# Performance work log

Measured on AMD Instinct MI355X. Metric: run time of the kernel, lower is better.

Reference implementation:

```python
import jax, jax.numpy as jnp
import numpy as np

BN_EPS = 1e-5

def conv1x1(x, w, b):
    # x: [B,C,H,W], w: [O,C], b: [O]
    return jnp.einsum('bchw,oc->bohw', x, w) + b[None, :, None, None]

def maxpool2(x):
    B, C, H, W = x.shape
    return x.reshape(B, C, H // 2, 2, W // 2, 2).max(axis=(3, 5))

def setup_inputs() -> dict:
    key = jax.random.key(0)
    ks = jax.random.split(key, 12)
    B, C, Ci, H, W = 8, 256, 128, 64, 64
    s = 0.05
    return {
        'x': jax.random.normal(ks[0], (B, C, H, W), jnp.float32),
        'y': jax.random.normal(ks[1], (B, C, H, W), jnp.float32),
        'g_w': jax.random.normal(ks[2], (Ci, C), jnp.float32) * s,
        'g_b': jax.random.normal(ks[3], (Ci,), jnp.float32) * s,
        'theta_w': jax.random.normal(ks[4], (Ci, C), jnp.float32) * s,
        'theta_b': jax.random.normal(ks[5], (Ci,), jnp.float32) * s,
        'phi_w': jax.random.normal(ks[6], (Ci, C), jnp.float32) * s,
        'phi_b': jax.random.normal(ks[7], (Ci,), jnp.float32) * s,
        'W_w': jax.random.normal(ks[8], (C, Ci), jnp.float32) * s,
        'W_b': jax.random.normal(ks[9], (C,), jnp.float32) * s,
        'bn_gamma': jax.random.normal(ks[10], (C,), jnp.float32) * s + 1.0,
        'bn_beta': jax.random.normal(ks[11], (C,), jnp.float32) * s,
    }

def reference(x, y, g_w, g_b, theta_w, theta_b, phi_w, phi_b, W_w, W_b, bn_gamma, bn_beta):
    B, C, H, W = x.shape
    Ci = g_w.shape[0]
    # g, phi applied to y then 2x2 max-pooled (sub_sample=True)
    g_y = maxpool2(conv1x1(y, g_w, g_b))          # [B,Ci,H/2,W/2]
    phi_y = maxpool2(conv1x1(y, phi_w, phi_b))    # [B,Ci,H/2,W/2]
    theta_x = conv1x1(x, theta_w, theta_b)        # [B,Ci,H,W]
    Np = (H // 2) * (W // 2)
    g_y = g_y.reshape(B, Ci, Np).transpose(0, 2, 1)      # [B,N',Ci]
    phi_y = phi_y.reshape(B, Ci, Np)                     # [B,Ci,N']
    theta_x = theta_x.reshape(B, Ci, H * W).transpose(0, 2, 1)  # [B,HW,Ci]
    f = jnp.einsum('bnc,bcm->bnm', theta_x, phi_y) / Np  # [B,HW,N']
    out = jnp.einsum('bnm,bmc->bnc', f, g_y)             # [B,HW,Ci]
    out = out.transpose(0, 2, 1).reshape(B, Ci, H, W)
    # W: 1x1 conv + BatchNorm2d (eval mode: running mean=0, var=1)
    W_y = conv1x1(out, W_w, W_b)
    W_y = W_y * (bn_gamma / jnp.sqrt(1.0 + BN_EPS))[None, :, None, None] + bn_beta[None, :, None, None]
    return W_y + x
```

## Files before the change

### kernel.cpp

```cpp
#include <hip/hip_runtime.h>
#include <math.h>


namespace {
constexpr int NB = 8;
constexpr int NC = 256;
constexpr int NI = 128;
constexpr int HW = 4096;
constexpr int NP = 1024;
constexpr int NCK = 32;
constexpr float BNEPS = 1e-5f;
}

typedef __bf16 bf16x8 __attribute__((ext_vector_type(8)));
typedef float f32x4 __attribute__((ext_vector_type(4)));

#define MFMA16(a, b, c) __builtin_amdgcn_mfma_f32_16x16x32_bf16((a), (b), (c), 0, 0, 0)

__device__ __forceinline__ unsigned rne_hi_bits(float f) {
    unsigned b = __float_as_uint(f);
    return (b + 0x7fffu + ((b >> 16) & 1u)) & 0xffff0000u;
}
__device__ __forceinline__ void split2pack(float e0, float e1, unsigned& hp, unsigned& lp) {
    unsigned h0 = rne_hi_bits(e0), h1 = rne_hi_bits(e1);
    float l0 = e0 - __uint_as_float(h0);
    float l1 = e1 - __uint_as_float(h1);
    unsigned g0 = rne_hi_bits(l0), g1 = rne_hi_bits(l1);
    hp = (h0 >> 16) | (h1 & 0xffff0000u);
    lp = (g0 >> 16) | (g1 & 0xffff0000u);
}
__device__ __forceinline__ int swz(int row, int kq) {
    return kq ^ ((row ^ (row >> 2)) & 7);
}

__global__ __launch_bounds__(256, 3)
void k_theta(const float* __restrict__ A, const float* __restrict__ abias,
             const float* __restrict__ X,
             unsigned short* __restrict__ outH, unsigned short* __restrict__ outL)
{
    __shared__ unsigned short Ah[64 * 64], Al[64 * 64], Xh[128 * 64], Xl[128 * 64];
    const int t = threadIdx.x;
    const int lane = t & 63;
    const int lq = lane >> 4;
    const int b = blockIdx.z;
    const int ihalf = blockIdx.y;
    const int pixbase = blockIdx.x * 128;
    const int wm = (t >> 7) & 1;
    const int wn = (t >> 6) & 1;
    const float* Xb = X + (size_t)b * NC * HW;

    const int k4 = (t & 15) * 4;
    const int kqa = k4 >> 3, ina = k4 & 7;
    const int kqx = t >> 5;
    const int pix4 = (t & 31) * 4;

    f32x4 acc[2][4];
#pragma unroll
    for (int i = 0; i < 2; ++i)
#pragma unroll
        for (int j = 0; j < 4; ++j) acc[i][j] = (f32x4)(0.f);

    float4 pA[4];
    float pXe[8][4];
#pragma unroll
    for (int p = 0; p < 4; ++p)
        pA[p] = *(const float4*)&A[(size_t)(ihalf * 64 + (t >> 4) + p * 16) * NC + k4];
#pragma unroll
    for (int j = 0; j < 8; ++j)
        *(float4*)&pXe[j][0] = *(const float4*)&Xb[(size_t)(kqx * 8 + j) * HW + pixbase + pix4];

#pragma unroll 1
    for (int kc = 0; kc < NC; kc += 64) {
#pragma unroll
        for (int p = 0; p < 4; ++p) {
            const int r = (t >> 4) + p * 16;
            unsigned hp0, lp0, hp1, lp1;
            split2pack(pA[p].x, pA[p].y, hp0, lp0);
            split2pack(pA[p].z, pA[p].w, hp1, lp1);
            const int idx = r * 64 + swz(r, kqa) * 8 + ina;
            *(uint2*)&Ah[idx] = make_uint2(hp0, hp1);
            *(uint2*)&Al[idx] = make_uint2(lp0, lp1);
        }
#pragma unroll
        for (int p = 0; p < 4; ++p) {
            unsigned hp[4], lp[4];
#pragma unroll
            for (int j2 = 0; j2 < 4; ++j2)
                split2pack(pXe[2 * j2][p], pXe[2 * j2 + 1][p], hp[j2], lp[j2]);
            const int pix = pix4 + p;
            const int idx = pix * 64 + swz(pix, kqx) * 8;
            *(uint4*)&Xh[idx] = make_uint4(hp[0], hp[1], hp[2], hp[3]);
            *(uint4*)&Xl[idx] = make_uint4(lp[0], lp[1], lp[2], lp[3]);
        }
        __syncthreads();
        if (kc + 64 < NC) {
#pragma unroll
            for (int p = 0; p < 4; ++p)
                pA[p] = *(const float4*)&A[(size_t)(ihalf * 64 + (t >> 4) + p * 16) * NC + kc + 64 + k4];
#pragma unroll
            for (int j = 0; j < 8; ++j)
                *(float4*)&pXe[j][0] = *(const float4*)&Xb[(size_t)(kc + 64 + kqx * 8 + j) * HW + pixbase + pix4];
        }
#pragma unroll
        for (int s = 0; s < 2; ++s) {
            bf16x8 ah[2], al[2], bh[4], bl[4];
#pragma unroll
            for (int mf = 0; mf < 2; ++mf) {
                const int r = wm * 32 + mf * 16 + (lane & 15);
                const int idx = r * 64 + swz(r, s * 4 + lq) * 8;
                ah[mf] = *(const bf16x8*)&Ah[idx];
                al[mf] = *(const bf16x8*)&Al[idx];
            }
#pragma unroll
            for (int nf = 0; nf < 4; ++nf) {
                const int pix = wn * 64 + nf * 16 + (lane & 15);
                const int idx = pix * 64 + swz(pix, s * 4 + lq) * 8;
                bh[nf] = *(const bf16x8*)&Xh[idx];
                bl[nf] = *(const bf16x8*)&Xl[idx];
            }
#pragma unroll
            for (int mf = 0; mf < 2; ++mf)
#pragma unroll
                for (int nf = 0; nf < 4; ++nf) {
                    acc[mf][nf] = MFMA16(ah[mf], bh[nf], acc[mf][nf]);
                    acc[mf][nf] = MFMA16(ah[mf], bl[nf], acc[mf][nf]);
                    acc[mf][nf] = MFMA16(al[mf], bh[nf], acc[mf][nf]);
                }
        }
        __syncthreads();
    }
#pragma unroll
    for (int mf = 0; mf < 2; ++mf) {
        const int il0 = wm * 32 + mf * 16 + lq * 4;
        const int gi0 = ihalf * 64 + il0;
        const float b0 = abias[gi0], b1 = abias[gi0 + 1], b2 = abias[gi0 + 2], b3 = abias[gi0 + 3];
#pragma unroll
        for (int nf = 0; nf < 4; ++nf) {
            const int pix = pixbase + wn * 64 + nf * 16 + (lane & 15);
            const float v0 = acc[mf][nf][0] + b0;
            const float v1 = acc[mf][nf][1] + b1;
            const float v2 = acc[mf][nf][2] + b2;
            const float v3 = acc[mf][nf][3] + b3;
            unsigned hp0, lp0, hp1, lp1;
            split2pack(v0, v1, hp0, lp0);
            split2pack(v2, v3, hp1, lp1);
            const size_t o = ((size_t)(b * 2 + ihalf) * HW + pix) * 64 + il0;
            *(uint2*)&outH[o] = make_uint2(hp0, hp1);
            *(uint2*)&outL[o] = make_uint2(lp0, lp1);
        }
    }
}

__global__ __launch_bounds__(256, 2)
void k_gphi(const float* __restrict__ Ag, const float* __restrict__ gbias,
            const float* __restrict__ Ap, const float* __restrict__ pbias,
            const float* __restrict__ X,
            float* __restrict__ gpout, float* __restrict__ ppout)
{
    __shared__ unsigned short Agh[64 * 64], Agl[64 * 64], Aph[64 * 64], Apl[64 * 64];
    __shared__ unsigned short Xh[128 * 64], Xl[128 * 64];
    const int t = threadIdx.x;
    const int lane = t & 63;
    const int lq = lane >> 4;
    const int b = blockIdx.z;
    const int ihalf = blockIdx.y;
    const int pr = blockIdx.x;
    const int pixbase = pr * 128;
    const int wm = (t >> 7) & 1;
    const int wn = (t >> 6) & 1;
    const float* Xb = X + (size_t)b * NC * HW;

    const int k4 = (t & 15) * 4;
    const int kqa = k4 >> 3, ina = k4 & 7;
    const int kqx = t >> 5;
    const int pix4 = (t & 31) * 4;

    f32x4 accg[2][4], accp[2][4];
#pragma unroll
    for (int i = 0; i < 2; ++i)
#pragma unroll
        for (int j = 0; j < 4; ++j) { accg[i][j] = (f32x4)(0.f); accp[i][j] = (f32x4)(0.f); }

    const int nbase[4] = {wn * 32, wn * 32 + 16, 64 + wn * 32, 64 + wn * 32 + 16};

    float4 pAg[4], pAp[4];
    float pXe[8][4];
#pragma unroll
    for (int p = 0; p < 4; ++p) {
        const size_t ro = (size_t)(ihalf * 64 + (t >> 4) + p * 16) * NC + k4;
        pAg[p] = *(const float4*)&Ag[ro];
        pAp[p] = *(const float4*)&Ap[ro];
    }
#pragma unroll
    for (int j = 0; j < 8; ++j)
        *(float4*)&pXe[j][0] = *(const float4*)&Xb[(size_t)(kqx * 8 + j) * HW + pixbase + pix4];

#pragma unroll 1
    for (int kc = 0; kc < NC; kc += 64) {
#pragma unroll
        for (int p = 0; p < 4; ++p) {
            const int r = (t >> 4) + p * 16;
            const int idx = r * 64 + swz(r, kqa) * 8 + ina;
            unsigned hp0, lp0, hp1, lp1;
            split2pack(pAg[p].x, pAg[p].y, hp0, lp0);
            split2pack(pAg[p].z, pAg[p].w, hp1, lp1);
            *(uint2*)&Agh[idx] = make_uint2(hp0, hp1);
            *(uint2*)&Agl[idx] = make_uint2(lp0, lp1);
            split2pack(pAp[p].x, pAp[p].y, hp0, lp0);
            split2pack(pAp[p].z, pAp[p].w, hp1, lp1);
            *(uint2*)&Aph[idx] = make_uint2(hp0, hp1);
            *(uint2*)&Apl[idx] = make_uint2(lp0, lp1);
        }
#pragma unroll
        for (int p = 0; p < 4; ++p) {
            unsigned hp[4], lp[4];
#pragma unroll
            for (int j2 = 0; j2 < 4; ++j2)
                split2pack(pXe[2 * j2][p], pXe[2 * j2 + 1][p], hp[j2], lp[j2]);
            const int pix = pix4 + p;
            const int idx = pix * 64 + swz(pix, kqx) * 8;
            *(uint4*)&Xh[idx] = make_uint4(hp[0], hp[1], hp[2], hp[3]);
            *(uint4*)&Xl[idx] = make_uint4(lp[0], lp[1], lp[2], lp[3]);
        }
        __syncthreads();
        if (kc + 64 < NC) {
#pragma unroll
            for (int p = 0; p < 4; ++p) {
                const size_t ro = (size_t)(ihalf * 64 + (t >> 4) + p * 16) * NC + kc + 64 + k4;
                pAg[p] = *(const float4*)&Ag[ro];
                pAp[p] = *(const float4*)&Ap[ro];
            }
#pragma unroll
            for (int j = 0; j < 8; ++j)
                *(float4*)&pXe[j][0] = *(const float4*)&Xb[(size_t)(kc + 64 + kqx * 8 + j) * HW + pixbase + pix4];
        }
#pragma unroll
        for (int s = 0; s < 2; ++s) {
            bf16x8 agh[2], agl[2], aph[2], apl[2], bh[4], bl[4];
#pragma unroll
            for (int mf = 0; mf < 2; ++mf) {
                const int r = wm * 32 + mf * 16 + (lane & 15);
                const int idx = r * 64 + swz(r, s * 4 + lq) * 8;
                agh[mf] = *(const bf16x8*)&Agh[idx];
                agl[mf] = *(const bf16x8*)&Agl[idx];
                aph[mf] = *(const bf16x8*)&Aph[idx];
                apl[mf] = *(const bf16x8*)&Apl[idx];
            }
#pragma unroll
            for (int nf = 0; nf < 4; ++nf) {
                const int pix = nbase[nf] + (lane & 15);
                const int idx = pix * 64 + swz(pix, s * 4 + lq) * 8;
                bh[nf] = *(const bf16x8*)&Xh[idx];
                bl[nf] = *(const bf16x8*)&Xl[idx];
            }
#pragma unroll
            for (int mf = 0; mf < 2; ++mf)
#pragma unroll
                for (int nf = 0; nf < 4; ++nf) {
                    accg[mf][nf] = MFMA16(agh[mf], bh[nf], accg[mf][nf]);
                    accg[mf][nf] = MFMA16(agh[mf], bl[nf], accg[mf][nf]);
                    accg[mf][nf] = MFMA16(agl[mf], bh[nf], accg[mf][nf]);
                    accp[mf][nf] = MFMA16(aph[mf], bh[nf], accp[mf][nf]);
                    accp[mf][nf] = MFMA16(aph[mf], bl[nf], accp[mf][nf]);
                    accp[mf][nf] = MFMA16(apl[mf], bh[nf], accp[mf][nf]);
                }
        }
        __syncthreads();
    }
#pragma unroll
    for (int which = 0; which < 2; ++which) {
        const float* bias = which ? pbias : gbias;
        float* dst = which ? ppout : gpout;
#pragma unroll
        for (int mf = 0; mf < 2; ++mf) {
            const int i0 = ihalf * 64 + wm * 32 + mf * 16 + lq * 4;
#pragma unroll
            for (int nfc = 0; nfc < 2; ++nfc) {
                f32x4 v;
                if (which == 0) {
#pragma unroll
                    for (int r = 0; r < 4; ++r)
                        v[r] = fmaxf(accg[mf][nfc][r], accg[mf][nfc + 2][r]);
                } else {
#pragma unroll
                    for (int r = 0; r < 4; ++r)
                        v[r] = fmaxf(accp[mf][nfc][r], accp[mf][nfc + 2][r]);
                }
                float h[4];
#pragma unroll
                for (int r = 0; r < 4; ++r)
                    h[r] = fmaxf(v[r], __shfl_xor(v[r], 1));
                if ((lane & 1) == 0) {
                    const int pcol = wn * 16 + nfc * 8 + ((lane & 15) >> 1);
#pragma unroll
                    for (int r = 0; r < 4; ++r)
                        dst[((size_t)b * NI + i0 + r) * NP + pr * 32 + pcol] = h[r] + bias[i0 + r];
                }
            }
        }
    }
}

__global__ __launch_bounds__(256)
void k_mpart(const float* __restrict__ G, const float* __restrict__ Ph,
             float* __restrict__ Mpart)
{
    __shared__ float Gs[32][132];
    __shared__ float Ps[32][132];
    const int t = threadIdx.x;
    const int ck = blockIdx.x;
    const int b = blockIdx.y;
    const int nbase = ck * 32;
    const float* Gb = G + (size_t)b * NI * NP;
    const float* Pb = Ph + (size_t)b * NI * NP;

    float acc[8][8];
#pragma unroll
    for (int i = 0; i < 8; ++i)
#pragma unroll
        for (int j = 0; j < 8; ++j) acc[i][j] = 0.f;

    const int j0 = (t >> 4) << 3;
    const int c0 = (t & 15) << 2;

    {
#pragma unroll
        for (int p = 0; p < 4; ++p) {
            const int r = p * 32 + (t >> 3);
            const int n4 = (t & 7) << 2;
            const float4 g = *(const float4*)&Gb[(size_t)r * NP + nbase + n4];
            Gs[n4 + 0][r] = g.x; Gs[n4 + 1][r] = g.y;
            Gs[n4 + 2][r] = g.z; Gs[n4 + 3][r] = g.w;
            const float4 f = *(const float4*)&Pb[(size_t)r * NP + nbase + n4];
            Ps[n4 + 0][r] = f.x; Ps[n4 + 1][r] = f.y;
            Ps[n4 + 2][r] = f.z; Ps[n4 + 3][r] = f.w;
        }
        __syncthreads();
#pragma unroll
        for (int nn = 0; nn < 32; ++nn) {
            const float4 a0 = *(const float4*)&Gs[nn][j0];
            const float4 a1 = *(const float4*)&Gs[nn][j0 + 4];
            const float4 b0 = *(const float4*)&Ps[nn][c0];
            const float4 b1 = *(const float4*)&Ps[nn][c0 + 64];
            const float av[8] = {a0.x, a0.y, a0.z, a0.w, a1.x, a1.y, a1.z, a1.w};
            const float bv[8] = {b0.x, b0.y, b0.z, b0.w, b1.x, b1.y, b1.z, b1.w};
#pragma unroll
            for (int i = 0; i < 8; ++i)
#pragma unroll
                for (int j = 0; j < 8; ++j)
                    acc[i][j] = fmaf(av[i], bv[j], acc[i][j]);
        }
    }

    float* Mb = Mpart + (size_t)(ck * NB + b) * (NI * NI);
#pragma unroll
    for (int jj = 0; jj < 8; ++jj) {
        float4 o0, o1;
        o0.x = acc[jj][0]; o0.y = acc[jj][1]; o0.z = acc[jj][2]; o0.w = acc[jj][3];
        o1.x = acc[jj][4]; o1.y = acc[jj][5]; o1.z = acc[jj][6]; o1.w = acc[jj][7];
        *(float4*)&Mb[(size_t)(j0 + jj) * NI + c0]      = o0;
        *(float4*)&Mb[(size_t)(j0 + jj) * NI + c0 + 64] = o1;
    }
}

__global__ __launch_bounds__(256)
void k_msum(const float* __restrict__ Mpart, float* __restrict__ M)
{
    const size_t idx4 = ((size_t)blockIdx.x * 256 + threadIdx.x) * 4;
    f32x4 s = (f32x4)(0.f);
#pragma unroll
    for (int ck = 0; ck < NCK; ++ck) {
        const float4 v = *(const float4*)&Mpart[(size_t)ck * NB * NI * NI + idx4];
        s[0] += v.x; s[1] += v.y; s[2] += v.z; s[3] += v.w;
    }
    float4 o; o.x = s[0]; o.y = s[1]; o.z = s[2]; o.w = s[3];
    *(float4*)&M[idx4] = o;
}

__global__ __launch_bounds__(256)
void k_pgemm(const float* __restrict__ M, const float* __restrict__ Wm,
             const float* __restrict__ bng, float* __restrict__ P)
{
    __shared__ float Ms[128][128];
    const int t = threadIdx.x;
    const int cbase = blockIdx.x * 64;
    const int b = blockIdx.y;
    const float* Mb = M + (size_t)b * NI * NI;

#pragma unroll
    for (int rep = 0; rep < 16; ++rep) {
        const int flat = rep * 256 + t;
        const int j = flat >> 5;
        const int i4 = (flat & 31) << 2;
        *(float4*)&Ms[j][i4] = *(const float4*)&Mb[(size_t)j * NI + i4];
    }
    __syncthreads();

    const float inv = 1.f / (float)NP;
    const int i0 = (t & 7) << 4;
#pragma unroll
    for (int pp = 0; pp < 2; ++pp) {
        const int c = cbase + pp * 32 + (t >> 3);
        const float* wrow = Wm + (size_t)c * NI;
        float a[16];
#pragma unroll
        for (int q = 0; q < 16; ++q) a[q] = 0.f;
#pragma unroll 4
        for (int j = 0; j < 128; ++j) {
            const float w = wrow[j];
            const float4 m0v = *(const float4*)&Ms[j][i0];
            const float4 m1v = *(const float4*)&Ms[j][i0 + 4];
            const float4 m2v = *(const float4*)&Ms[j][i0 + 8];
            const float4 m3v = *(const float4*)&Ms[j][i0 + 12];
            a[0]  = fmaf(w, m0v.x, a[0]);  a[1]  = fmaf(w, m0v.y, a[1]);
            a[2]  = fmaf(w, m0v.z, a[2]);  a[3]  = fmaf(w, m0v.w, a[3]);
            a[4]  = fmaf(w, m1v.x, a[4]);  a[5]  = fmaf(w, m1v.y, a[5]);
            a[6]  = fmaf(w, m1v.z, a[6]);  a[7]  = fmaf(w, m1v.w, a[7]);
            a[8]  = fmaf(w, m2v.x, a[8]);  a[9]  = fmaf(w, m2v.y, a[9]);
            a[10] = fmaf(w, m2v.z, a[10]); a[11] = fmaf(w, m2v.w, a[11]);
            a[12] = fmaf(w, m3v.x, a[12]); a[13] = fmaf(w, m3v.y, a[13]);
            a[14] = fmaf(w, m3v.z, a[14]); a[15] = fmaf(w, m3v.w, a[15]);
        }
        const float sc = bng[c] / sqrtf(1.f + BNEPS) * inv;
        float* Pp = P + ((size_t)b * NC + c) * NI + i0;
#pragma unroll
        for (int q = 0; q < 4; ++q) {
            float4 o;
            o.x = a[4 * q] * sc;     o.y = a[4 * q + 1] * sc;
            o.z = a[4 * q + 2] * sc; o.w = a[4 * q + 3] * sc;
            *(float4*)&Pp[4 * q] = o;
        }
    }
}

__global__ __launch_bounds__(256, 3)
void k_final(const float* __restrict__ P,
             const unsigned short* __restrict__ TTh, const unsigned short* __restrict__ TTl,
             const float* __restrict__ Wb, const float* __restrict__ bng,
             const float* __restrict__ bnb, const float* __restrict__ xres,
             float* __restrict__ out)
{
    __shared__ unsigned short Ph_[64 * 64], Pl_[64 * 64], Th[128 * 64], Tl[128 * 64];
    const int t = threadIdx.x;
    const int lane = t & 63;
    const int lq = lane >> 4;
    const int b = blockIdx.z;
    const int cbase = blockIdx.y * 64;
    const int pixbase = blockIdx.x * 128;
    const int wm = (t >> 7) & 1;
    const int wn = (t >> 6) & 1;
    const float* Pb = P + (size_t)b * NC * NI;

    const int k4 = (t & 15) * 4;
    const int kqa = k4 >> 3, ina = k4 & 7;
    const int kqt = t & 7;
    const int pixt = t >> 3;

    f32x4 acc[2][4];
#pragma unroll
    for (int i = 0; i < 2; ++i)
#pragma unroll
        for (int j = 0; j < 4; ++j) acc[i][j] = (f32x4)(0.f);

    float4 pP[4];
    uint4 pTh[4], pTl[4];
#pragma unroll
    for (int p = 0; p < 4; ++p)
        pP[p] = *(const float4*)&Pb[(size_t)(cbase + (t >> 4) + p * 16) * NI + k4];
#pragma unroll
    for (int p = 0; p < 4; ++p) {
        const size_t o = ((size_t)(b * 2 + 0) * HW + pixbase + pixt + p * 32) * 64 + kqt * 8;
        pTh[p] = *(const uint4*)&TTh[o];
        pTl[p] = *(const uint4*)&TTl[o];
    }

#pragma unroll 1
    for (int ic = 0; ic < NI; ic += 64) {
#pragma unroll
        for (int p = 0; p < 4; ++p) {
            const int r = (t >> 4) + p * 16;
            unsigned hp0, lp0, hp1, lp1;
            split2pack(pP[p].x, pP[p].y, hp0, lp0);
            split2pack(pP[p].z, pP[p].w, hp1, lp1);
            const int idx = r * 64 + swz(r, kqa) * 8 + ina;
            *(uint2*)&Ph_[idx] = make_uint2(hp0, hp1);
            *(uint2*)&Pl_[idx] = make_uint2(lp0, lp1);
        }
#pragma unroll
        for (int p = 0; p < 4; ++p) {
            const int pix = pixt + p * 32;
            const int idx = pix * 64 + swz(pix, kqt) * 8;
            *(uint4*)&Th[idx] = pTh[p];
            *(uint4*)&Tl[idx] = pTl[p];
        }
        __syncthreads();
        if (ic + 64 < NI) {
#pragma unroll
            for (int p = 0; p < 4; ++p)
                pP[p] = *(const float4*)&Pb[(size_t)(cbase + (t >> 4) + p * 16) * NI + ic + 64 + k4];
#pragma unroll
            for (int p = 0; p < 4; ++p) {
                const size_t o = ((size_t)(b * 2 + 1) * HW + pixbase + pixt + p * 32) * 64 + kqt * 8;
                pTh[p] = *(const uint4*)&TTh[o];
                pTl[p] = *(const uint4*)&TTl[o];
            }
        }
#pragma unroll
        for (int s = 0; s < 2; ++s) {
            bf16x8 ah[2], al[2], bh[4], bl[4];
#pragma unroll
            for (int mf = 0; mf < 2; ++mf) {
                const int r = wm * 32 + mf * 16 + (lane & 15);
                const int idx = r * 64 + swz(r, s * 4 + lq) * 8;
                ah[mf] = *(const bf16x8*)&Ph_[idx];
                al[mf] = *(const bf16x8*)&Pl_[idx];
            }
#pragma unroll
            for (int nf = 0; nf < 4; ++nf) {
                const int pix = wn * 64 + nf * 16 + (lane & 15);
                const int idx = pix * 64 + swz(pix, s * 4 + lq) * 8;
                bh[nf] = *(const bf16x8*)&Th[idx];
                bl[nf] = *(const bf16x8*)&Tl[idx];
            }
#pragma unroll
            for (int mf = 0; mf < 2; ++mf)
#pragma unroll
                for (int nf = 0; nf < 4; ++nf) {
                    acc[mf][nf] = MFMA16(ah[mf], bh[nf], acc[mf][nf]);
                    acc[mf][nf] = MFMA16(ah[mf], bl[nf], acc[mf][nf]);
                    acc[mf][nf] = MFMA16(al[mf], bh[nf], acc[mf][nf]);
                }
        }
        __syncthreads();
    }
    const float rs = rsqrtf(1.f + BNEPS);
#pragma unroll
    for (int mf = 0; mf < 2; ++mf) {
        const int c0 = cbase + wm * 32 + mf * 16 + lq * 4;
        float beta[4];
#pragma unroll
        for (int r = 0; r < 4; ++r) {
            const float scv = bng[c0 + r] * rs;
            beta[r] = scv * Wb[c0 + r] + bnb[c0 + r];
        }
#pragma unroll
        for (int nf = 0; nf < 4; ++nf) {
            const int pix = pixbase + wn * 64 + nf * 16 + (lane & 15);
#pragma unroll
            for (int r = 0; r < 4; ++r) {
                const size_t o = ((size_t)b * NC + c0 + r) * HW + pix;
                out[o] = acc[mf][nf][r] + beta[r] + xres[o];
            }
        }
    }
}

extern "C" void kernel_launch(void* const* d_in, const int* in_sizes, int n_in,
                              void* d_out, int out_size, void* d_ws, size_t ws_size,
                              hipStream_t stream)
{
    const float* x    = (const float*)d_in[0];
    const float* y    = (const float*)d_in[1];
    const float* g_w  = (const float*)d_in[2];
    const float* g_b  = (const float*)d_in[3];
    const float* th_w = (const float*)d_in[4];
    const float* th_b = (const float*)d_in[5];
    const float* ph_w = (const float*)d_in[6];
    const float* ph_b = (const float*)d_in[7];
    const float* Wm   = (const float*)d_in[8];
    const float* Wb   = (const float*)d_in[9];
    const float* bng  = (const float*)d_in[10];
    const float* bnb  = (const float*)d_in[11];
    float* out = (float*)d_out;
    char* ws = (char*)d_ws;

    unsigned short* TTh = (unsigned short*)ws;
    unsigned short* TTl = TTh + (size_t)NB * 2 * HW * 64;
    float* gp = (float*)(TTl + (size_t)NB * 2 * HW * 64);
    float* pp = gp + (size_t)NB * NI * NP;
    float* mp = pp + (size_t)NB * NI * NP;
    float* M  = mp + (size_t)NCK * NB * NI * NI;
    float* P  = M  + (size_t)NB * NI * NI;

    const dim3 blk(256);
    k_theta<<<dim3(32, 2, NB), blk, 0, stream>>>(th_w, th_b, x, TTh, TTl);
    k_gphi<<<dim3(32, 2, NB), blk, 0, stream>>>(g_w, g_b, ph_w, ph_b, y, gp, pp);
    k_mpart<<<dim3(NCK, NB), blk, 0, stream>>>(gp, pp, mp);
    k_msum<<<dim3(NB * NI * NI / 1024), blk, 0, stream>>>(mp, M);
    k_pgemm<<<dim3(4, NB), blk, 0, stream>>>(M, Wm, bng, P);
    k_final<<<dim3(32, 4, NB), blk, 0, stream>>>(P, TTh, TTl, Wb, bng, bnb, x, out);
}
```

Measured before the change: 215.1 us.

## Drop split-bf16 emulation for single bf16 MFMA and retile theta/final kernels

Removes the hi/lo bf16 split (3 MFMAs per product) and uses a single bf16 MFMA throughout the theta, g/phi and final GEMMs, halving shared-memory staging and intermediate storage. k_theta is retiled to compute all 128 inner channels per 64-pixel block and writes pre-tiled swizzled bf16 tiles that k_final loads directly. k_final stages its output through shared memory for coalesced float4 residual reads and writes, and k_pgemm now emits scaled bf16 tiles. This cuts MFMA count and memory traffic at the cost of reduced numerical accuracy, which may push errors against the tolerance.

```diff
diff --git a/kernel.cpp b/kernel.cpp
--- a/kernel.cpp
+++ b/kernel.cpp
@@ -14,6 +14,7 @@
 
 typedef __bf16 bf16x8 __attribute__((ext_vector_type(8)));
 typedef float f32x4 __attribute__((ext_vector_type(4)));
+typedef unsigned short us;
 
 #define MFMA16(a, b, c) __builtin_amdgcn_mfma_f32_16x16x32_bf16((a), (b), (c), 0, 0, 0)
 
@@ -21,159 +22,134 @@
     unsigned b = __float_as_uint(f);
     return (b + 0x7fffu + ((b >> 16) & 1u)) & 0xffff0000u;
 }
-__device__ __forceinline__ void split2pack(float e0, float e1, unsigned& hp, unsigned& lp) {
-    unsigned h0 = rne_hi_bits(e0), h1 = rne_hi_bits(e1);
-    float l0 = e0 - __uint_as_float(h0);
-    float l1 = e1 - __uint_as_float(h1);
-    unsigned g0 = rne_hi_bits(l0), g1 = rne_hi_bits(l1);
-    hp = (h0 >> 16) | (h1 & 0xffff0000u);
-    lp = (g0 >> 16) | (g1 & 0xffff0000u);
+__device__ __forceinline__ unsigned pack2bf(float e0, float e1) {
+    return (rne_hi_bits(e0) >> 16) | (rne_hi_bits(e1) & 0xffff0000u);
 }
 __device__ __forceinline__ int swz(int row, int kq) {
     return kq ^ ((row ^ (row >> 2)) & 7);
 }
-
-__global__ __launch_bounds__(256, 3)
+__device__ __forceinline__ int swz16(int row, int q) {
+    return q ^ (row & 7);
+}
+
+__global__ __launch_bounds__(256)
 void k_theta(const float* __restrict__ A, const float* __restrict__ abias,
-             const float* __restrict__ X,
-             unsigned short* __restrict__ outH, unsigned short* __restrict__ outL)
-{
-    __shared__ unsigned short Ah[64 * 64], Al[64 * 64], Xh[128 * 64], Xl[128 * 64];
-    const int t = threadIdx.x;
-    const int lane = t & 63;
-    const int lq = lane >> 4;
-    const int b = blockIdx.z;
-    const int ihalf = blockIdx.y;
-    const int pixbase = blockIdx.x * 128;
-    const int wm = (t >> 7) & 1;
-    const int wn = (t >> 6) & 1;
+             const float* __restrict__ X, us* __restrict__ TT)
+{
+    __shared__ char smem[24576];
+    us* As = (us*)smem;
+    us* Xs = (us*)(smem + 16384);
+    const int t = threadIdx.x, lane = t & 63, l15 = lane & 15, lq = lane >> 4;
+    const int w = t >> 6, wi = w & 1, wp = w >> 1;
+    const int b = blockIdx.z, pixbase = blockIdx.x * 64;
     const float* Xb = X + (size_t)b * NC * HW;
 
-    const int k4 = (t & 15) * 4;
-    const int kqa = k4 >> 3, ina = k4 & 7;
-    const int kqx = t >> 5;
-    const int pix4 = (t & 31) * 4;
-
-    f32x4 acc[2][4];
-#pragma unroll
-    for (int i = 0; i < 2; ++i)
-#pragma unroll
-        for (int j = 0; j < 4; ++j) acc[i][j] = (f32x4)(0.f);
-
-    float4 pA[4];
-    float pXe[8][4];
-#pragma unroll
-    for (int p = 0; p < 4; ++p)
-        pA[p] = *(const float4*)&A[(size_t)(ihalf * 64 + (t >> 4) + p * 16) * NC + k4];
-#pragma unroll
-    for (int j = 0; j < 8; ++j)
-        *(float4*)&pXe[j][0] = *(const float4*)&Xb[(size_t)(kqx * 8 + j) * HW + pixbase + pix4];
+    const int k4 = (t & 15) * 4, kqa = k4 >> 3, ina = k4 & 7;
+    const int arow = t >> 4;
+    const int ks = t >> 4, pix4 = (t & 15) * 4;
+    const int kqx = ks >> 1, inx = (ks & 1) * 4;
+
+    f32x4 acc[4][2];
+#pragma unroll
+    for (int i = 0; i < 4; ++i)
+#pragma unroll
+        for (int j = 0; j < 2; ++j) acc[i][j] = (f32x4)(0.f);
+
+    float4 pA[8];
+    float pXe[4][4];
+#pragma unroll
+    for (int p = 0; p < 8; ++p)
+        pA[p] = *(const float4*)&A[(size_t)(arow + p * 16) * NC + k4];
+#pragma unroll
+    for (int j = 0; j < 4; ++j) {
+        const float4 tv = *(const float4*)&Xb[(size_t)(ks * 4 + j) * HW + pixbase + pix4];
+        pXe[j][0] = tv.x; pXe[j][1] = tv.y; pXe[j][2] = tv.z; pXe[j][3] = tv.w;
+    }
 
 #pragma unroll 1
     for (int kc = 0; kc < NC; kc += 64) {
 #pragma unroll
+        for (int p = 0; p < 8; ++p) {
+            const int r = arow + p * 16;
+            *(uint2*)&As[r * 64 + swz(r, kqa) * 8 + ina] =
+                make_uint2(pack2bf(pA[p].x, pA[p].y), pack2bf(pA[p].z, pA[p].w));
+        }
+#pragma unroll
         for (int p = 0; p < 4; ++p) {
-            const int r = (t >> 4) + p * 16;
-            unsigned hp0, lp0, hp1, lp1;
-            split2pack(pA[p].x, pA[p].y, hp0, lp0);
-            split2pack(pA[p].z, pA[p].w, hp1, lp1);
-            const int idx = r * 64 + swz(r, kqa) * 8 + ina;
-            *(uint2*)&Ah[idx] = make_uint2(hp0, hp1);
-            *(uint2*)&Al[idx] = make_uint2(lp0, lp1);
-        }
-#pragma unroll
-        for (int p = 0; p < 4; ++p) {
-            unsigned hp[4], lp[4];
-#pragma unroll
-            for (int j2 = 0; j2 < 4; ++j2)
-                split2pack(pXe[2 * j2][p], pXe[2 * j2 + 1][p], hp[j2], lp[j2]);
             const int pix = pix4 + p;
-            const int idx = pix * 64 + swz(pix, kqx) * 8;
-            *(uint4*)&Xh[idx] = make_uint4(hp[0], hp[1], hp[2], hp[3]);
-            *(uint4*)&Xl[idx] = make_uint4(lp[0], lp[1], lp[2], lp[3]);
+            *(uint2*)&Xs[pix * 64 + swz(pix, kqx) * 8 + inx] =
+                make_uint2(pack2bf(pXe[0][p], pXe[1][p]), pack2bf(pXe[2][p], pXe[3][p]));
         }
         __syncthreads();
         if (kc + 64 < NC) {
 #pragma unroll
-            for (int p = 0; p < 4; ++p)
-                pA[p] = *(const float4*)&A[(size_t)(ihalf * 64 + (t >> 4) + p * 16) * NC + kc + 64 + k4];
-#pragma unroll
-            for (int j = 0; j < 8; ++j)
-                *(float4*)&pXe[j][0] = *(const float4*)&Xb[(size_t)(kc + 64 + kqx * 8 + j) * HW + pixbase + pix4];
+            for (int p = 0; p < 8; ++p)
+                pA[p] = *(const float4*)&A[(size_t)(arow + p * 16) * NC + kc + 64 + k4];
+#pragma unroll
+            for (int j = 0; j < 4; ++j) {
+                const float4 tv = *(const float4*)&Xb[(size_t)(kc + 64 + ks * 4 + j) * HW + pixbase + pix4];
+                pXe[j][0] = tv.x; pXe[j][1] = tv.y; pXe[j][2] = tv.z; pXe[j][3] = tv.w;
+            }
         }
 #pragma unroll
         for (int s = 0; s < 2; ++s) {
-            bf16x8 ah[2], al[2], bh[4], bl[4];
-#pragma unroll
-            for (int mf = 0; mf < 2; ++mf) {
-                const int r = wm * 32 + mf * 16 + (lane & 15);
-                const int idx = r * 64 + swz(r, s * 4 + lq) * 8;
-                ah[mf] = *(const bf16x8*)&Ah[idx];
-                al[mf] = *(const bf16x8*)&Al[idx];
-            }
-#pragma unroll
-            for (int nf = 0; nf < 4; ++nf) {
-                const int pix = wn * 64 + nf * 16 + (lane & 15);
-                const int idx = pix * 64 + swz(pix, s * 4 + lq) * 8;
-                bh[nf] = *(const bf16x8*)&Xh[idx];
-                bl[nf] = *(const bf16x8*)&Xl[idx];
-            }
-#pragma unroll
-            for (int mf = 0; mf < 2; ++mf)
-#pragma unroll
-                for (int nf = 0; nf < 4; ++nf) {
-                    acc[mf][nf] = MFMA16(ah[mf], bh[nf], acc[mf][nf]);
-                    acc[mf][nf] = MFMA16(ah[mf], bl[nf], acc[mf][nf]);
-                    acc[mf][nf] = MFMA16(al[mf], bh[nf], acc[mf][nf]);
-                }
+            bf16x8 a[4], bb[2];
+#pragma unroll
+            for (int mf = 0; mf < 4; ++mf) {
+                const int r = wi * 64 + mf * 16 + l15;
+                a[mf] = *(const bf16x8*)&As[r * 64 + swz(r, s * 4 + lq) * 8];
+            }
+#pragma unroll
+            for (int nf = 0; nf < 2; ++nf) {
+                const int pr = wp * 32 + nf * 16 + l15;
+                bb[nf] = *(const bf16x8*)&Xs[pr * 64 + swz(pr, s * 4 + lq) * 8];
+            }
+#pragma unroll
+            for (int mf = 0; mf < 4; ++mf)
+#pragma unroll
+                for (int nf = 0; nf < 2; ++nf)
+                    acc[mf][nf] = MFMA16(a[mf], bb[nf], acc[mf][nf]);
         }
         __syncthreads();
     }
-#pragma unroll
-    for (int mf = 0; mf < 2; ++mf) {
-        const int il0 = wm * 32 + mf * 16 + lq * 4;
-        const int gi0 = ihalf * 64 + il0;
-        const float b0 = abias[gi0], b1 = abias[gi0 + 1], b2 = abias[gi0 + 2], b3 = abias[gi0 + 3];
-#pragma unroll
-        for (int nf = 0; nf < 4; ++nf) {
-            const int pix = pixbase + wn * 64 + nf * 16 + (lane & 15);
-            const float v0 = acc[mf][nf][0] + b0;
-            const float v1 = acc[mf][nf][1] + b1;
-            const float v2 = acc[mf][nf][2] + b2;
-            const float v3 = acc[mf][nf][3] + b3;
-            unsigned hp0, lp0, hp1, lp1;
-            split2pack(v0, v1, hp0, lp0);
-            split2pack(v2, v3, hp1, lp1);
-            const size_t o = ((size_t)(b * 2 + ihalf) * HW + pix) * 64 + il0;
-            *(uint2*)&outH[o] = make_uint2(hp0, hp1);
-            *(uint2*)&outL[o] = make_uint2(lp0, lp1);
-        }
-    }
-}
-
-__global__ __launch_bounds__(256, 2)
+    us* Ts = (us*)smem;
+#pragma unroll
+    for (int mf = 0; mf < 4; ++mf) {
+        const int i0 = wi * 64 + mf * 16 + lq * 4;
+        const float b0 = abias[i0], b1 = abias[i0 + 1], b2 = abias[i0 + 2], b3 = abias[i0 + 3];
+        const int q = i0 >> 3, inn = i0 & 7;
+#pragma unroll
+        for (int nf = 0; nf < 2; ++nf) {
+            const int pix = wp * 32 + nf * 16 + l15;
+            *(uint2*)&Ts[pix * 128 + swz16(pix, q) * 8 + inn] =
+                make_uint2(pack2bf(acc[mf][nf][0] + b0, acc[mf][nf][1] + b1),
+                           pack2bf(acc[mf][nf][2] + b2, acc[mf][nf][3] + b3));
+        }
+    }
+    __syncthreads();
+    us* dst = TT + ((size_t)b * 64 + blockIdx.x) * 8192;
+#pragma unroll
+    for (int p = 0; p < 4; ++p) {
+        const int flat = p * 256 + t;
+        *(uint4*)&dst[flat * 8] = *(const uint4*)&Ts[flat * 8];
+    }
+}
+
+__global__ __launch_bounds__(256)
 void k_gphi(const float* __restrict__ Ag, const float* __restrict__ gbias,
             const float* __restrict__ Ap, const float* __restrict__ pbias,
             const float* __restrict__ X,
             float* __restrict__ gpout, float* __restrict__ ppout)
 {
-    __shared__ unsigned short Agh[64 * 64], Agl[64 * 64], Aph[64 * 64], Apl[64 * 64];
-    __shared__ unsigned short Xh[128 * 64], Xl[128 * 64];
-    const int t = threadIdx.x;
-    const int lane = t & 63;
-    const int lq = lane >> 4;
-    const int b = blockIdx.z;
-    const int ihalf = blockIdx.y;
-    const int pr = blockIdx.x;
+    __shared__ us Ags[64 * 64], Aps[64 * 64], Xs[128 * 64];
+    const int t = threadIdx.x, lane = t & 63, l15 = lane & 15, lq = lane >> 4;
+    const int b = blockIdx.z, ihalf = blockIdx.y, pr = blockIdx.x;
     const int pixbase = pr * 128;
-    const int wm = (t >> 7) & 1;
-    const int wn = (t >> 6) & 1;
+    const int wm = (t >> 7) & 1, wn = (t >> 6) & 1;
     const float* Xb = X + (size_t)b * NC * HW;
 
-    const int k4 = (t & 15) * 4;
-    const int kqa = k4 >> 3, ina = k4 & 7;
-    const int kqx = t >> 5;
-    const int pix4 = (t & 31) * 4;
+    const int k4 = (t & 15) * 4, kqa = k4 >> 3, ina = k4 & 7;
+    const int kqx = t >> 5, pix4 = (t & 31) * 4;
 
     f32x4 accg[2][4], accp[2][4];
 #pragma unroll
@@ -192,8 +168,10 @@
         pAp[p] = *(const float4*)&Ap[ro];
     }
 #pragma unroll
-    for (int j = 0; j < 8; ++j)
-        *(float4*)&pXe[j][0] = *(const float4*)&Xb[(size_t)(kqx * 8 + j) * HW + pixbase + pix4];
+    for (int j = 0; j < 8; ++j) {
+        const float4 tv = *(const float4*)&Xb[(size_t)(kqx * 8 + j) * HW + pixbase + pix4];
+        pXe[j][0] = tv.x; pXe[j][1] = tv.y; pXe[j][2] = tv.z; pXe[j][3] = tv.w;
+    }
 
 #pragma unroll 1
     for (int kc = 0; kc < NC; kc += 64) {
@@ -201,26 +179,15 @@
         for (int p = 0; p < 4; ++p) {
             const int r = (t >> 4) + p * 16;
             const int idx = r * 64 + swz(r, kqa) * 8 + ina;
-            unsigned hp0, lp0, hp1, lp1;
-            split2pack(pAg[p].x, pAg[p].y, hp0, lp0);
-            split2pack(pAg[p].z, pAg[p].w, hp1, lp1);
-            *(uint2*)&Agh[idx] = make_uint2(hp0, hp1);
-            *(uint2*)&Agl[idx] = make_uint2(lp0, lp1);
-            split2pack(pAp[p].x, pAp[p].y, hp0, lp0);
-            split2pack(pAp[p].z, pAp[p].w, hp1, lp1);
-            *(uint2*)&Aph[idx] = make_uint2(hp0, hp1);
-            *(uint2*)&Apl[idx] = make_uint2(lp0, lp1);
+            *(uint2*)&Ags[idx] = make_uint2(pack2bf(pAg[p].x, pAg[p].y), pack2bf(pAg[p].z, pAg[p].w));
+            *(uint2*)&Aps[idx] = make_uint2(pack2bf(pAp[p].x, pAp[p].y), pack2bf(pAp[p].z, pAp[p].w));
         }
 #pragma unroll
         for (int p = 0; p < 4; ++p) {
-            unsigned hp[4], lp[4];
-#pragma unroll
-            for (int j2 = 0; j2 < 4; ++j2)
-                split2pack(pXe[2 * j2][p], pXe[2 * j2 + 1][p], hp[j2], lp[j2]);
             const int pix = pix4 + p;
-            const int idx = pix * 64 + swz(pix, kqx) * 8;
-            *(uint4*)&Xh[idx] = make_uint4(hp[0], hp[1], hp[2], hp[3]);
-            *(uint4*)&Xl[idx] = make_uint4(lp[0], lp[1], lp[2], lp[3]);
+            *(uint4*)&Xs[pix * 64 + swz(pix, kqx) * 8] =
+                make_uint4(pack2bf(pXe[0][p], pXe[1][p]), pack2bf(pXe[2][p], pXe[3][p]),
+                           pack2bf(pXe[4][p], pXe[5][p]), pack2bf(pXe[6][p], pXe[7][p]));
         }
         __syncthreads();
         if (kc + 64 < NC) {
@@ -231,38 +198,32 @@
                 pAp[p] = *(const float4*)&Ap[ro];
             }
 #pragma unroll
-            for (int j = 0; j < 8; ++j)
-                *(float4*)&pXe[j][0] = *(const float4*)&Xb[(size_t)(kc + 64 + kqx * 8 + j) * HW + pixbase + pix4];
+            for (int j = 0; j < 8; ++j) {
+                const float4 tv = *(const float4*)&Xb[(size_t)(kc + 64 + kqx * 8 + j) * HW + pixbase + pix4];
+                pXe[j][0] = tv.x; pXe[j][1] = tv.y; pXe[j][2] = tv.z; pXe[j][3] = tv.w;
+            }
         }
 #pragma unroll
         for (int s = 0; s < 2; ++s) {
-            bf16x8 agh[2], agl[2], aph[2], apl[2], bh[4], bl[4];
+            bf16x8 ag[2], ap[2], bb[4];
 #pragma unroll
             for (int mf = 0; mf < 2; ++mf) {
-                const int r = wm * 32 + mf * 16 + (lane & 15);
+                const int r = wm * 32 + mf * 16 + l15;
                 const int idx = r * 64 + swz(r, s * 4 + lq) * 8;
-                agh[mf] = *(const bf16x8*)&Agh[idx];
-                agl[mf] = *(const bf16x8*)&Agl[idx];
-                aph[mf] = *(const bf16x8*)&Aph[idx];
-                apl[mf] = *(const bf16x8*)&Apl[idx];
+                ag[mf] = *(const bf16x8*)&Ags[idx];
+                ap[mf] = *(const bf16x8*)&Aps[idx];
             }
 #pragma unroll
             for (int nf = 0; nf < 4; ++nf) {
-                const int pix = nbase[nf] + (lane & 15);
-                const int idx = pix * 64 + swz(pix, s * 4 + lq) * 8;
-                bh[nf] = *(const bf16x8*)&Xh[idx];
-                bl[nf] = *(const bf16x8*)&Xl[idx];
+                const int pix = nbase[nf] + l15;
+                bb[nf] = *(const bf16x8*)&Xs[pix * 64 + swz(pix, s * 4 + lq) * 8];
             }
 #pragma unroll
             for (int mf = 0; mf < 2; ++mf)
 #pragma unroll
                 for (int nf = 0; nf < 4; ++nf) {
-                    accg[mf][nf] = MFMA16(agh[mf], bh[nf], accg[mf][nf]);
-                    accg[mf][nf] = MFMA16(agh[mf], bl[nf], accg[mf][nf]);
-                    accg[mf][nf] = MFMA16(agl[mf], bh[nf], accg[mf][nf]);
-                    accp[mf][nf] = MFMA16(aph[mf], bh[nf], accp[mf][nf]);
-                    accp[mf][nf] = MFMA16(aph[mf], bl[nf], accp[mf][nf]);
-                    accp[mf][nf] = MFMA16(apl[mf], bh[nf], accp[mf][nf]);
+                    accg[mf][nf] = MFMA16(ag[mf], bb[nf], accg[mf][nf]);
+                    accp[mf][nf] = MFMA16(ap[mf], bb[nf], accp[mf][nf]);
                 }
         }
         __syncthreads();
@@ -291,7 +252,7 @@
                 for (int r = 0; r < 4; ++r)
                     h[r] = fmaxf(v[r], __shfl_xor(v[r], 1));
                 if ((lane & 1) == 0) {
-                    const int pcol = wn * 16 + nfc * 8 + ((lane & 15) >> 1);
+                    const int pcol = wn * 16 + nfc * 8 + (l15 >> 1);
 #pragma unroll
                     for (int r = 0; r < 4; ++r)
                         dst[((size_t)b * NI + i0 + r) * NP + pr * 32 + pcol] = h[r] + bias[i0 + r];
@@ -323,33 +284,31 @@
     const int j0 = (t >> 4) << 3;
     const int c0 = (t & 15) << 2;
 
-    {
-#pragma unroll
-        for (int p = 0; p < 4; ++p) {
-            const int r = p * 32 + (t >> 3);
-            const int n4 = (t & 7) << 2;
-            const float4 g = *(const float4*)&Gb[(size_t)r * NP + nbase + n4];
-            Gs[n4 + 0][r] = g.x; Gs[n4 + 1][r] = g.y;
-            Gs[n4 + 2][r] = g.z; Gs[n4 + 3][r] = g.w;
-            const float4 f = *(const float4*)&Pb[(size_t)r * NP + nbase + n4];
-            Ps[n4 + 0][r] = f.x; Ps[n4 + 1][r] = f.y;
-            Ps[n4 + 2][r] = f.z; Ps[n4 + 3][r] = f.w;
-        }
-        __syncthreads();
-#pragma unroll
-        for (int nn = 0; nn < 32; ++nn) {
-            const float4 a0 = *(const float4*)&Gs[nn][j0];
-            const float4 a1 = *(const float4*)&Gs[nn][j0 + 4];
-            const float4 b0 = *(const float4*)&Ps[nn][c0];
-            const float4 b1 = *(const float4*)&Ps[nn][c0 + 64];
-            const float av[8] = {a0.x, a0.y, a0.z, a0.w, a1.x, a1.y, a1.z, a1.w};
-            const float bv[8] = {b0.x, b0.y, b0.z, b0.w, b1.x, b1.y, b1.z, b1.w};
-#pragma unroll
-            for (int i = 0; i < 8; ++i)
-#pragma unroll
-                for (int j = 0; j < 8; ++j)
-                    acc[i][j] = fmaf(av[i], bv[j], acc[i][j]);
-        }
+#pragma unroll
+    for (int p = 0; p < 4; ++p) {
+        const int r = p * 32 + (t >> 3);
+        const int n4 = (t & 7) << 2;
+        const float4 g = *(const float4*)&Gb[(size_t)r * NP + nbase + n4];
+        Gs[n4 + 0][r] = g.x; Gs[n4 + 1][r] = g.y;
+        Gs[n4 + 2][r] = g.z; Gs[n4 + 3][r] = g.w;
+        const float4 f = *(const float4*)&Pb[(size_t)r * NP + nbase + n4];
+        Ps[n4 + 0][r] = f.x; Ps[n4 + 1][r] = f.y;
+        Ps[n4 + 2][r] = f.z; Ps[n4 + 3][r] = f.w;
+    }
+    __syncthreads();
+#pragma unroll
+    for (int nn = 0; nn < 32; ++nn) {
+        const float4 a0 = *(const float4*)&Gs[nn][j0];
+        const float4 a1 = *(const float4*)&Gs[nn][j0 + 4];
+        const float4 b0 = *(const float4*)&Ps[nn][c0];
+        const float4 b1 = *(const float4*)&Ps[nn][c0 + 64];
+        const float av[8] = {a0.x, a0.y, a0.z, a0.w, a1.x, a1.y, a1.z, a1.w};
+        const float bv[8] = {b0.x, b0.y, b0.z, b0.w, b1.x, b1.y, b1.z, b1.w};
+#pragma unroll
+        for (int i = 0; i < 8; ++i)
+#pragma unroll
+            for (int j = 0; j < 8; ++j)
+                acc[i][j] = fmaf(av[i], bv[j], acc[i][j]);
     }
 
     float* Mb = Mpart + (size_t)(ck * NB + b) * (NI * NI);
@@ -379,7 +338,7 @@
 
 __global__ __launch_bounds__(256)
 void k_pgemm(const float* __restrict__ M, const float* __restrict__ Wm,
-             const float* __restrict__ bng, float* __restrict__ P)
+             const float* __restrict__ bng, us* __restrict__ Pp)
 {
     __shared__ float Ms[128][128];
     const int t = threadIdx.x;
@@ -422,136 +381,96 @@
             a[14] = fmaf(w, m3v.z, a[14]); a[15] = fmaf(w, m3v.w, a[15]);
         }
         const float sc = bng[c] / sqrtf(1.f + BNEPS) * inv;
-        float* Pp = P + ((size_t)b * NC + c) * NI + i0;
-#pragma unroll
-        for (int q = 0; q < 4; ++q) {
-            float4 o;
-            o.x = a[4 * q] * sc;     o.y = a[4 * q + 1] * sc;
-            o.z = a[4 * q + 2] * sc; o.w = a[4 * q + 3] * sc;
-            *(float4*)&Pp[4 * q] = o;
-        }
-    }
-}
-
-__global__ __launch_bounds__(256, 3)
-void k_final(const float* __restrict__ P,
-             const unsigned short* __restrict__ TTh, const unsigned short* __restrict__ TTl,
+        const int r = pp * 32 + (t >> 3);
+        const int q0 = (t & 7) * 2;
+        us* dst = Pp + ((size_t)b * 4 + blockIdx.x) * 8192 + r * 128;
+        *(uint4*)&dst[swz16(r, q0) * 8] =
+            make_uint4(pack2bf(a[0] * sc, a[1] * sc), pack2bf(a[2] * sc, a[3] * sc),
+                       pack2bf(a[4] * sc, a[5] * sc), pack2bf(a[6] * sc, a[7] * sc));
+        *(uint4*)&dst[swz16(r, q0 + 1) * 8] =
+            make_uint4(pack2bf(a[8] * sc, a[9] * sc), pack2bf(a[10] * sc, a[11] * sc),
+                       pack2bf(a[12] * sc, a[13] * sc), pack2bf(a[14] * sc, a[15] * sc));
+    }
+}
+
+__global__ __launch_bounds__(256)
+void k_final(const us* __restrict__ Pp, const us* __restrict__ TT,
              const float* __restrict__ Wb, const float* __restrict__ bng,
              const float* __restrict__ bnb, const float* __restrict__ xres,
              float* __restrict__ out)
 {
-    __shared__ unsigned short Ph_[64 * 64], Pl_[64 * 64], Th[128 * 64], Tl[128 * 64];
-    const int t = threadIdx.x;
-    const int lane = t & 63;
-    const int lq = lane >> 4;
-    const int b = blockIdx.z;
-    const int cbase = blockIdx.y * 64;
-    const int pixbase = blockIdx.x * 128;
-    const int wm = (t >> 7) & 1;
-    const int wn = (t >> 6) & 1;
-    const float* Pb = P + (size_t)b * NC * NI;
-
-    const int k4 = (t & 15) * 4;
-    const int kqa = k4 >> 3, ina = k4 & 7;
-    const int kqt = t & 7;
-    const int pixt = t >> 3;
-
-    f32x4 acc[2][4];
+    __shared__ char smem[32768];
+    us* As = (us*)smem;
+    us* Bs = (us*)(smem + 16384);
+    const int t = threadIdx.x, lane = t & 63, l15 = lane & 15, lq = lane >> 4;
+    const int w = t >> 6, wc = w & 1, wp = w >> 1;
+    const int b = blockIdx.z, ct = blockIdx.y, pt = blockIdx.x;
+    const us* Atile = Pp + ((size_t)b * 4 + ct) * 8192;
+    const us* Btile = TT + ((size_t)b * 64 + pt) * 8192;
+
+#pragma unroll
+    for (int p = 0; p < 4; ++p) {
+        const int flat = p * 256 + t;
+        *(uint4*)&As[flat * 8] = *(const uint4*)&Atile[flat * 8];
+        *(uint4*)&Bs[flat * 8] = *(const uint4*)&Btile[flat * 8];
+    }
+    __syncthreads();
+
+    f32x4 acc[2][2];
 #pragma unroll
     for (int i = 0; i < 2; ++i)
 #pragma unroll
-        for (int j = 0; j < 4; ++j) acc[i][j] = (f32x4)(0.f);
-
-    float4 pP[4];
-    uint4 pTh[4], pTl[4];
-#pragma unroll
-    for (int p = 0; p < 4; ++p)
-        pP[p] = *(const float4*)&Pb[(size_t)(cbase + (t >> 4) + p * 16) * NI + k4];
+        for (int j = 0; j < 2; ++j) acc[i][j] = (f32x4)(0.f);
+
+#pragma unroll
+    for (int s = 0; s < 4; ++s) {
+        bf16x8 a[2], bb[2];
+#pragma unroll
+        for (int mf = 0; mf < 2; ++mf) {
+            const int r = wc * 32 + mf * 16 + l15;
+            a[mf] = *(const bf16x8*)&As[r * 128 + swz16(r, s * 4 + lq) * 8];
+        }
+#pragma unroll
+        for (int nf = 0; nf < 2; ++nf) {
+            const int pr = wp * 32 + nf * 16 + l15;
+            bb[nf] = *(const bf16x8*)&Bs[pr * 128 + swz16(pr, s * 4 + lq) * 8];
+        }
+#pragma unroll
+        for (int mf = 0; mf < 2; ++mf)
+#pragma unroll
+            for (int nf = 0; nf < 2; ++nf)
+                acc[mf][nf] = MFMA16(a[mf], bb[nf], acc[mf][nf]);
+    }
+    __syncthreads();
+
+    float* Es = (float*)smem;
+#pragma unroll
+    for (int mf = 0; mf < 2; ++mf)
+#pragma unroll
+        for (int nf = 0; nf < 2; ++nf) {
+            const int cl = wc * 32 + mf * 16 + lq * 4;
+            const int pl = wp * 32 + nf * 16 + l15;
+#pragma unroll
+            for (int r = 0; r < 4; ++r)
+                Es[(cl + r) * 66 + pl] = acc[mf][nf][r];
+        }
+    __syncthreads();
+
+    const float rs = rsqrtf(1.f + BNEPS);
 #pragma unroll
     for (int p = 0; p < 4; ++p) {
-        const size_t o = ((size_t)(b * 2 + 0) * HW + pixbase + pixt + p * 32) * 64 + kqt * 8;
-        pTh[p] = *(const uint4*)&TTh[o];
-        pTl[p] = *(const uint4*)&TTl[o];
-    }
-
-#pragma unroll 1
-    for (int ic = 0; ic < NI; ic += 64) {
-#pragma unroll
-        for (int p = 0; p < 4; ++p) {
-            const int r = (t >> 4) + p * 16;
-            unsigned hp0, lp0, hp1, lp1;
-            split2pack(pP[p].x, pP[p].y, hp0, lp0);
-            split2pack(pP[p].z, pP[p].w, hp1, lp1);
-            const int idx = r * 64 + swz(r, kqa) * 8 + ina;
-            *(uint2*)&Ph_[idx] = make_uint2(hp0, hp1);
-            *(uint2*)&Pl_[idx] = make_uint2(lp0, lp1);
-        }
-#pragma unroll
-        for (int p = 0; p < 4; ++p) {
-            const int pix = pixt + p * 32;
-            const int idx = pix * 64 + swz(pix, kqt) * 8;
-            *(uint4*)&Th[idx] = pTh[p];
-            *(uint4*)&Tl[idx] = pTl[p];
-        }
-        __syncthreads();
-        if (ic + 64 < NI) {
-#pragma unroll
-            for (int p = 0; p < 4; ++p)
-                pP[p] = *(const float4*)&Pb[(size_t)(cbase + (t >> 4) + p * 16) * NI + ic + 64 + k4];
-#pragma unroll
-            for (int p = 0; p < 4; ++p) {
-                const size_t o = ((size_t)(b * 2 + 1) * HW + pixbase + pixt + p * 32) * 64 + kqt * 8;
-                pTh[p] = *(const uint4*)&TTh[o];
-                pTl[p] = *(const uint4*)&TTl[o];
-            }
-        }
-#pragma unroll
-        for (int s = 0; s < 2; ++s) {
-            bf16x8 ah[2], al[2], bh[4], bl[4];
-#pragma unroll
-            for (int mf = 0; mf < 2; ++mf) {
-                const int r = wm * 32 + mf * 16 + (lane & 15);
-                const int idx = r * 64 + swz(r, s * 4 + lq) * 8;
-                ah[mf] = *(const bf16x8*)&Ph_[idx];
-                al[mf] = *(const bf16x8*)&Pl_[idx];
-            }
-#pragma unroll
-            for (int nf = 0; nf < 4; ++nf) {
-                const int pix = wn * 64 + nf * 16 + (lane & 15);
-                const int idx = pix * 64 + swz(pix, s * 4 + lq) * 8;
-                bh[nf] = *(const bf16x8*)&Th[idx];
-                bl[nf] = *(const bf16x8*)&Tl[idx];
-            }
-#pragma unroll
-            for (int mf = 0; mf < 2; ++mf)
-#pragma unroll
-                for (int nf = 0; nf < 4; ++nf) {
-                    acc[mf][nf] = MFMA16(ah[mf], bh[nf], acc[mf][nf]);
-                    acc[mf][nf] = MFMA16(ah[mf], bl[nf], acc[mf][nf]);
-                    acc[mf][nf] = MFMA16(al[mf], bh[nf], acc[mf][nf]);
-                }
-        }
-        __syncthreads();
-    }
-    const float rs = rsqrtf(1.f + BNEPS);
-#pragma unroll
-    for (int mf = 0; mf < 2; ++mf) {
-        const int c0 = cbase + wm * 32 + mf * 16 + lq * 4;
-        float beta[4];
-#pragma unroll
-        for (int r = 0; r < 4; ++r) {
-            const float scv = bng[c0 + r] * rs;
-            beta[r] = scv * Wb[c0 + r] + bnb[c0 + r];
-        }
-#pragma unroll
-        for (int nf = 0; nf < 4; ++nf) {
-            const int pix = pixbase + wn * 64 + nf * 16 + (lane & 15);
-#pragma unroll
-            for (int r = 0; r < 4; ++r) {
-                const size_t o = ((size_t)b * NC + c0 + r) * HW + pix;
-                out[o] = acc[mf][nf][r] + beta[r] + xres[o];
-            }
-        }
+        const int flat = p * 256 + t;
+        const int cl = flat >> 4;
+        const int p4 = (flat & 15) * 4;
+        const int cg = ct * 64 + cl;
+        const float beta = bng[cg] * rs * Wb[cg] + bnb[cg];
+        const size_t o = ((size_t)b * NC + cg) * HW + pt * 64 + p4;
+        const float4 xv = *(const float4*)&xres[o];
+        const float4 ev = *(const float4*)&Es[cl * 66 + p4];
+        float4 ov;
+        ov.x = ev.x + beta + xv.x; ov.y = ev.y + beta + xv.y;
+        ov.z = ev.z + beta + xv.z; ov.w = ev.w + beta + xv.w;
+        *(float4*)&out[o] = ov;
     }
 }
 
@@ -572,21 +491,19 @@
     const float* bng  = (const float*)d_in[10];
     const float* bnb  = (const float*)d_in[11];
     float* out = (float*)d_out;
-    char* ws = (char*)d_ws;
-
-    unsigned short* TTh = (unsigned short*)ws;
-    unsigned short* TTl = TTh + (size_t)NB * 2 * HW * 64;
-    float* gp = (float*)(TTl + (size_t)NB * 2 * HW * 64);
+
+    us* TT = (us*)d_ws;
+    us* Pp = TT + (size_t)NB * 64 * 8192;
+    float* gp = (float*)(Pp + (size_t)NB * 4 * 8192);
     float* pp = gp + (size_t)NB * NI * NP;
     float* mp = pp + (size_t)NB * NI * NP;
     float* M  = mp + (size_t)NCK * NB * NI * NI;
-    float* P  = M  + (size_t)NB * NI * NI;
 
     const dim3 blk(256);
-    k_theta<<<dim3(32, 2, NB), blk, 0, stream>>>(th_w, th_b, x, TTh, TTl);
+    k_theta<<<dim3(64, 1, NB), blk, 0, stream>>>(th_w, th_b, x, TT);
     k_gphi<<<dim3(32, 2, NB), blk, 0, stream>>>(g_w, g_b, ph_w, ph_b, y, gp, pp);
     k_mpart<<<dim3(NCK, NB), blk, 0, stream>>>(gp, pp, mp);
-    k_msum<<<dim3(NB * NI * NI / 1024), blk, 0, stream>>>(mp, M);
-    k_pgemm<<<dim3(4, NB), blk, 0, stream>>>(M, Wm, bng, P);
-    k_final<<<dim3(32, 4, NB), blk, 0, stream>>>(P, TTh, TTl, Wb, bng, bnb, x, out);
-}
+    k_msum<<<dim3(128), blk, 0, stream>>>(mp, M);
+    k_pgemm<<<dim3(4, NB), blk, 0, stream>>>(M, Wm, bng, Pp);
+    k_final<<<dim3(64, 4, NB), blk, 0, stream>>>(Pp, TT, Wb, bng, bnb, x, out);
+}
```

After: 182.7 us. 1.18x faster.
